# Optimization experiments

Measured on AMD Instinct MI355X. Metric: run time of the kernel, lower is better.

The kernel has to match this reference:

```python
import jax, jax.numpy as jnp
import numpy as np

# FP4 (e2m1) value table: sign bit in code>>3, magnitude in code&7
FP4 = jnp.array([0.0, 0.5, 1.0, 1.5, 2.0, 3.0, 4.0, 6.0,
                 -0.0, -0.5, -1.0, -1.5, -2.0, -3.0, -4.0, -6.0], dtype=jnp.float32)
BLOCK = 32  # MX block size: one shared E8M0 scale per 32 elements


def _unpack(packed):
    # packed: int32 holding byte values 0..255; low nibble first
    lo = packed & 0xF
    hi = (packed >> 4) & 0xF
    return jnp.stack([lo, hi], axis=-1).reshape(*packed.shape[:-1], packed.shape[-1] * 2)


def _dequant(packed, sf):
    # packed: [..., N//2] packed FP4 codes; sf: [..., N//32] E8M0 exponents
    vals = FP4[_unpack(packed)]                       # [..., N]
    n = vals.shape[-1]
    scale = jnp.exp2(sf.astype(jnp.float32) - 127.0)  # [..., N//32]
    vals = vals.reshape(*vals.shape[:-1], n // BLOCK, BLOCK) * scale[..., None]
    return vals.reshape(*scale.shape[:-1], n)


def setup_inputs() -> dict:
    key = jax.random.key(0)
    ks = jax.random.split(key, 6)
    M, IN, OUT, R = 8192, 4096, 4096, 128
    return {
        "x_q": jax.random.randint(ks[0], (M, IN // 2), 0, 256, dtype=jnp.int32),
        "scales_x": jax.random.randint(ks[1], (M, IN // BLOCK), 120, 134, dtype=jnp.int32),
        "weight": jax.random.randint(ks[2], (OUT, IN // 2), 0, 256, dtype=jnp.int32),
        "SF_w": jax.random.randint(ks[3], (OUT * IN // BLOCK,), 120, 134, dtype=jnp.int32),
        "low_rank_weight": jax.random.randint(ks[4], (OUT, R // 2), 0, 256, dtype=jnp.int32),
        "SF_low_rank_weight": jax.random.randint(ks[5], (OUT * R // BLOCK,), 120, 134, dtype=jnp.int32),
    }


def reference(x_q, scales_x, weight, SF_w, low_rank_weight, SF_low_rank_weight):
    OUT = weight.shape[0]
    IN = weight.shape[1] * 2
    R = low_rank_weight.shape[1] * 2  # 128
    # Low-rank path: first R unpacked features of x (R//2 packed bytes, R//32 scale blocks)
    x_lr = _dequant(x_q[:, :R // 2], scales_x[:, :R // BLOCK])                    # [M, R]
    W_lr = _dequant(low_rank_weight, SF_low_rank_weight.reshape(OUT, R // BLOCK))  # [OUT, R]
    out = jnp.einsum('mr,or->mo', x_lr, W_lr, preferred_element_type=jnp.float32)
    # Main 4-bit matmul fused with the low-rank correction
    x = _dequant(x_q, scales_x)                               # [M, IN]
    W = _dequant(weight, SF_w.reshape(OUT, IN // BLOCK))      # [OUT, IN]
    out = out + jnp.einsum('mi,oi->mo', x, W, preferred_element_type=jnp.float32)
    return out
```

## Files before the change

kernel.cpp:

```cpp
#include <hip/hip_runtime.h>
#include <hip/hip_bf16.h>
#include <stdint.h>


#define M_DIM 8192
#define N_DIM 4096
#define K_MAIN 4096
#define K_TOT 4224
#define KB_TOT 2112
#define NT 33

#define XE_OFF   ((size_t)0)
#define WE_OFF   (XE_OFF + (size_t)M_DIM * KB_TOT)
#define SXH_OFF  (WE_OFF + (size_t)N_DIM * KB_TOT)
#define SWH_OFF  (SXH_OFF + (size_t)NT * 2 * M_DIM * 2)
#define WS_NEED  (SWH_OFF + (size_t)NT * 2 * N_DIM * 2)

typedef __attribute__((ext_vector_type(4))) float f32x4;
typedef __attribute__((ext_vector_type(16))) float f32x16;
typedef __attribute__((ext_vector_type(8))) short short8;
typedef __attribute__((ext_vector_type(8))) _Float16 half8;
typedef __attribute__((ext_vector_type(4))) int i32x4;
typedef __attribute__((ext_vector_type(8))) int i32x8;

#define PX_N  (M_DIM * (KB_TOT / 4))
#define PW_N  (N_DIM * (KB_TOT / 4))
#define TSX_N (NT * 2 * M_DIM / 2)
#define TSW_N (NT * 2 * N_DIM / 2)
#define PACK_TOTAL (PX_N + PW_N + TSX_N + TSW_N)

__global__ __launch_bounds__(256)
void pack_kernel(const int* __restrict__ xq, const int* __restrict__ sx,
                 const int* __restrict__ w, const int* __restrict__ sfw,
                 const int* __restrict__ lrw, const int* __restrict__ sflr,
                 uint8_t* __restrict__ ws) {
    int t = blockIdx.x * 256 + threadIdx.x;
    if (t < PX_N) {
        int row = t / (KB_TOT / 4);
        int j = (t % (KB_TOT / 4)) * 4;
        int jsrc = (j < 2048) ? j : (j - 2048);
        i32x4 q = *(const i32x4*)(xq + (size_t)row * 2048 + jsrc);
        unsigned v = (q.x & 255) | ((q.y & 255) << 8) | ((q.z & 255) << 16) |
                     ((unsigned)(q.w & 255) << 24);
        *(unsigned*)(ws + XE_OFF + (size_t)row * KB_TOT + j) = v;
    } else if (t < PX_N + PW_N) {
        int i = t - PX_N;
        int row = i / (KB_TOT / 4);
        int j = (i % (KB_TOT / 4)) * 4;
        i32x4 q;
        if (j < 2048) q = *(const i32x4*)(w + (size_t)row * 2048 + j);
        else          q = *(const i32x4*)(lrw + (size_t)row * 64 + (j - 2048));
        unsigned v = (q.x & 255) | ((q.y & 255) << 8) | ((q.z & 255) << 16) |
                     ((unsigned)(q.w & 255) << 24);
        *(unsigned*)(ws + WE_OFF + (size_t)row * KB_TOT + j) = v;
    } else if (t < PX_N + PW_N + TSX_N) {
        int i = t - PX_N - PW_N;
        int plane = i >> 12;
        int kt = plane >> 1, h = plane & 1;
        int r2 = (i & 4095) << 1;
        int g0 = kt * 4 + h, g2 = g0 + 2;
        int s0 = (g0 < 128) ? g0 : g0 - 128;
        int s2 = (g2 < 128) ? g2 : g2 - 128;
        unsigned b0 = sx[(size_t)r2 * 128 + s0] & 255;
        unsigned b1 = sx[(size_t)r2 * 128 + s2] & 255;
        unsigned b2 = sx[(size_t)(r2 + 1) * 128 + s0] & 255;
        unsigned b3 = sx[(size_t)(r2 + 1) * 128 + s2] & 255;
        *(unsigned*)(ws + SXH_OFF + (size_t)i * 4) = b0 | (b1 << 8) | (b2 << 16) | (b3 << 24);
    } else if (t < PACK_TOTAL) {
        int i = t - PX_N - PW_N - TSX_N;
        int plane = i >> 11;
        int kt = plane >> 1, h = plane & 1;
        int r2 = (i & 2047) << 1;
        int g0 = kt * 4 + h, g2 = g0 + 2;
        unsigned b0, b1, b2, b3;
        if (g0 < 128) { b0 = sfw[(size_t)r2 * 128 + g0] & 255; b2 = sfw[(size_t)(r2 + 1) * 128 + g0] & 255; }
        else          { b0 = sflr[(size_t)r2 * 4 + (g0 - 128)] & 255; b2 = sflr[(size_t)(r2 + 1) * 4 + (g0 - 128)] & 255; }
        if (g2 < 128) { b1 = sfw[(size_t)r2 * 128 + g2] & 255; b3 = sfw[(size_t)(r2 + 1) * 128 + g2] & 255; }
        else          { b1 = sflr[(size_t)r2 * 4 + (g2 - 128)] & 255; b3 = sflr[(size_t)(r2 + 1) * 4 + (g2 - 128)] & 255; }
        *(unsigned*)(ws + SWH_OFF + (size_t)i * 4) = b0 | (b1 << 8) | (b2 << 16) | (b3 << 24);
    }
}

__device__ inline void gload_lds16(const void* g, void* l) {
    __builtin_amdgcn_global_load_lds(
        (const __attribute__((address_space(1))) unsigned int*)g,
        (__attribute__((address_space(3))) unsigned int*)l, 16, 0, 0);
}

__device__ inline void stage_tile(const uint8_t* __restrict__ xe,
                                  const uint8_t* __restrict__ we,
                                  int bm, int bn, int tt,
                                  uint8_t (*As)[256][16], uint8_t (*Bs)[256][16],
                                  int wid, int lane) {
    if (wid < 4) {
        const int c = wid;
        const uint8_t* g = xe + (size_t)(bm + lane) * KB_TOT + tt * 64 + c * 16;
#pragma unroll
        for (int q = 0; q < 4; ++q)
            gload_lds16(g + (size_t)q * 64 * KB_TOT, &As[c][q * 64][0]);
    } else {
        const int c = wid - 4;
        const uint8_t* g = we + (size_t)(bn + lane) * KB_TOT + tt * 64 + c * 16;
#pragma unroll
        for (int q = 0; q < 4; ++q)
            gload_lds16(g + (size_t)q * 64 * KB_TOT, &Bs[c][q * 64][0]);
    }
}

__device__ inline void load_scales(const uint8_t* __restrict__ sxH,
                                   const uint8_t* __restrict__ swH,
                                   int bm, int bn, int tt, int* sa, int* sb,
                                   int wr, int wc, int lane) {
    const int h = lane >> 5, r = lane & 31;
    const uint8_t* px = sxH + (size_t)((tt * 2 + h) * M_DIM + bm + wr * 128 + r) * 2;
#pragma unroll
    for (int mi = 0; mi < 4; ++mi) sa[mi] = *(const unsigned short*)(px + mi * 64);
    const uint8_t* pw = swH + (size_t)((tt * 2 + h) * N_DIM + bn + wc * 64 + r) * 2;
#pragma unroll
    for (int ni = 0; ni < 2; ++ni) sb[ni] = *(const unsigned short*)(pw + ni * 64);
}

template <int KK>
__device__ inline void compute_phase(const uint8_t (*As)[256][16],
                                     const uint8_t (*Bs)[256][16],
                                     f32x16 (&acc)[4][2], const int* sa, const int* sb,
                                     int wr, int wc, int lane) {
    const int h = lane >> 5, r = lane & 31;
    const int c = KK * 2 + h;
    i32x4 af[4], bf[2];
#pragma unroll
    for (int mi = 0; mi < 4; ++mi)
        af[mi] = *(const i32x4*)&As[c][wr * 128 + mi * 32 + r][0];
#pragma unroll
    for (int ni = 0; ni < 2; ++ni)
        bf[ni] = *(const i32x4*)&Bs[c][wc * 64 + ni * 32 + r][0];
    __builtin_amdgcn_s_setprio(1);
#pragma unroll
    for (int mi = 0; mi < 4; ++mi)
#pragma unroll
        for (int ni = 0; ni < 2; ++ni) {
            i32x8 a8 = {af[mi].x, af[mi].y, af[mi].z, af[mi].w, 0, 0, 0, 0};
            i32x8 b8 = {bf[ni].x, bf[ni].y, bf[ni].z, bf[ni].w, 0, 0, 0, 0};
            acc[mi][ni] = __builtin_amdgcn_mfma_scale_f32_32x32x64_f8f6f4(
                a8, b8, acc[mi][ni], 4, 4, KK, sa[mi], KK, sb[ni]);
        }
    __builtin_amdgcn_s_setprio(0);
}

__global__ __launch_bounds__(512, 2)
void l4b_mx2(const uint8_t* __restrict__ xe, const uint8_t* __restrict__ we,
             const uint8_t* __restrict__ sxH, const uint8_t* __restrict__ swH,
             float* __restrict__ out) {
    __shared__ __align__(16) uint8_t As[2][4][256][16];
    __shared__ __align__(16) uint8_t Bs[2][4][256][16];

    const int tid = threadIdx.x;
    const int lane = tid & 63;
    const int wid = tid >> 6;
    const int wr = wid >> 2;
    const int wc = wid & 3;

    const int bid = blockIdx.x;
    const int wgid = (bid & 7) * 64 + (bid >> 3);
    const int bm = (wgid & 31) * 256;
    const int bn = (wgid >> 5) * 256;

    f32x16 acc[4][2] = {};
    int sa[4], sb[2], san[4], sbn[2];

    stage_tile(xe, we, bm, bn, 0, As[0], Bs[0], wid, lane);
    load_scales(sxH, swH, bm, bn, 0, sa, sb, wr, wc, lane);
    __syncthreads();

    int cur = 0;
    for (int t = 0; t < NT - 1; ++t) {
        const int nxt = cur ^ 1;
        stage_tile(xe, we, bm, bn, t + 1, As[nxt], Bs[nxt], wid, lane);
        load_scales(sxH, swH, bm, bn, t + 1, san, sbn, wr, wc, lane);
        compute_phase<0>(As[cur], Bs[cur], acc, sa, sb, wr, wc, lane);
        compute_phase<1>(As[cur], Bs[cur], acc, sa, sb, wr, wc, lane);
        __syncthreads();
        cur = nxt;
#pragma unroll
        for (int i = 0; i < 4; ++i) sa[i] = san[i];
        sb[0] = sbn[0]; sb[1] = sbn[1];
    }
    compute_phase<0>(As[cur], Bs[cur], acc, sa, sb, wr, wc, lane);
    compute_phase<1>(As[cur], Bs[cur], acc, sa, sb, wr, wc, lane);

#pragma unroll
    for (int mi = 0; mi < 4; ++mi)
#pragma unroll
        for (int ni = 0; ni < 2; ++ni) {
            const int col = bn + wc * 64 + ni * 32 + (lane & 31);
            const int rb = bm + wr * 128 + mi * 32 + 4 * (lane >> 5);
#pragma unroll
            for (int reg = 0; reg < 16; ++reg) {
                const int row = rb + (reg & 3) + 8 * (reg >> 2);
                out[(size_t)row * N_DIM + col] = acc[mi][ni][reg];
            }
        }
}

__device__ inline short8 dequant8_f16(i32x4 q, int sf) {
    unsigned b = (unsigned)q.x | ((unsigned)q.y << 8) |
                 ((unsigned)q.z << 16) | ((unsigned)q.w << 24);
    unsigned me = b & 0x07070707u;
    unsigned mo = (b >> 4) & 0x07070707u;
    const unsigned TLO = 0x3E3C3800u;
    const unsigned THI = 0x46444240u;
    unsigned He = __builtin_amdgcn_perm(THI, TLO, me);
    unsigned Ho = __builtin_amdgcn_perm(THI, TLO, mo);
    He |= (b & 0x08080808u) << 4;
    Ho |= (b & 0x80808080u);
    unsigned d0 = __builtin_amdgcn_perm(He, 0u, 0x05010400u);
    unsigned d1 = __builtin_amdgcn_perm(He, 0u, 0x07000600u);
    unsigned d2 = __builtin_amdgcn_perm(Ho, 0u, 0x05010400u);
    unsigned d3 = __builtin_amdgcn_perm(Ho, 0u, 0x07000600u);
    i32x4 di; di.x = (int)d0; di.y = (int)d1; di.z = (int)d2; di.w = (int)d3;
    half8 hh = __builtin_bit_cast(half8, di);
    unsigned short se = (unsigned short)((sf - 112) << 10);
    int srep = (int)((unsigned)se | ((unsigned)se << 16));
    i32x4 si; si.x = srep; si.y = srep; si.z = srep; si.w = srep;
    hh = hh * __builtin_bit_cast(half8, si);
    return __builtin_bit_cast(short8, hh);
}

__global__ __launch_bounds__(256)
void l4b_fused(const int* __restrict__ x_q, const int* __restrict__ scales_x,
               const int* __restrict__ weight, const int* __restrict__ SF_w,
               const int* __restrict__ lrw, const int* __restrict__ SF_lr,
               float* __restrict__ out) {
    __shared__ short As[128 * 64];
    __shared__ short Bs[128 * 64];
    const int tid = threadIdx.x;
    const int lane = tid & 63;
    const int wid = tid >> 6;
    const int wr = wid >> 1, wc = wid & 1;
    const int bm = blockIdx.y * 128, bn = blockIdx.x * 128;
    const int srow = tid >> 3;
    const int scol = (tid & 7) * 8;
    f32x4 acc[4][4] = {};
    for (int kt = 0; kt < K_TOT / 64; ++kt) {
        const int k0 = kt * 64;
        __syncthreads();
#pragma unroll
        for (int it = 0; it < 4; ++it) {
            const int row = it * 32 + srow;
            const int k = k0 + scol;
            const int ksrc = (k < K_MAIN) ? k : (k - K_MAIN);
            i32x4 q = *(const i32x4*)(x_q + (size_t)(bm + row) * 2048 + (ksrc >> 1));
            int sf = scales_x[(size_t)(bm + row) * 128 + (ksrc >> 5)];
            short8 v = dequant8_f16(q, sf);
            unsigned a = (unsigned)(row * 128 + scol * 2) ^ (unsigned)((row & 7) << 4);
            *(short8*)((char*)As + a) = v;
        }
#pragma unroll
        for (int it = 0; it < 4; ++it) {
            const int row = it * 32 + srow;
            const int k = k0 + scol;
            i32x4 q; int sf;
            if (k < K_MAIN) {
                q = *(const i32x4*)(weight + (size_t)(bn + row) * 2048 + (k >> 1));
                sf = SF_w[(size_t)(bn + row) * 128 + (k >> 5)];
            } else {
                q = *(const i32x4*)(lrw + (size_t)(bn + row) * 64 + ((k - K_MAIN) >> 1));
                sf = SF_lr[(size_t)(bn + row) * 4 + ((k - K_MAIN) >> 5)];
            }
            short8 v = dequant8_f16(q, sf);
            unsigned a = (unsigned)(row * 128 + scol * 2) ^ (unsigned)((row & 7) << 4);
            *(short8*)((char*)Bs + a) = v;
        }
        __syncthreads();
#pragma unroll
        for (int ks = 0; ks < 2; ++ks) {
            const int koff = ks * 32 + (lane >> 4) * 8;
            short8 af[4], bfr[4];
#pragma unroll
            for (int mi = 0; mi < 4; ++mi) {
                const int row = wr * 64 + mi * 16 + (lane & 15);
                unsigned a = (unsigned)(row * 128 + koff * 2) ^ (unsigned)((row & 7) << 4);
                af[mi] = *(const short8*)((const char*)As + a);
            }
#pragma unroll
            for (int ni = 0; ni < 4; ++ni) {
                const int row = wc * 64 + ni * 16 + (lane & 15);
                unsigned a = (unsigned)(row * 128 + koff * 2) ^ (unsigned)((row & 7) << 4);
                bfr[ni] = *(const short8*)((const char*)Bs + a);
            }
#pragma unroll
            for (int mi = 0; mi < 4; ++mi)
#pragma unroll
                for (int ni = 0; ni < 4; ++ni)
                    acc[mi][ni] = __builtin_amdgcn_mfma_f32_16x16x32_f16(
                        __builtin_bit_cast(half8, af[mi]),
                        __builtin_bit_cast(half8, bfr[ni]),
                        acc[mi][ni], 0, 0, 0);
        }
    }
#pragma unroll
    for (int mi = 0; mi < 4; ++mi)
#pragma unroll
        for (int ni = 0; ni < 4; ++ni) {
            const int col = bn + wc * 64 + ni * 16 + (lane & 15);
            const int row0 = bm + wr * 64 + mi * 16 + (lane >> 4) * 4;
#pragma unroll
            for (int r2 = 0; r2 < 4; ++r2)
                out[(size_t)(row0 + r2) * N_DIM + col] = acc[mi][ni][r2];
        }
}

extern "C" void kernel_launch(void* const* d_in, const int* in_sizes, int n_in,
                              void* d_out, int out_size, void* d_ws, size_t ws_size,
                              hipStream_t stream) {
    const int* x_q  = (const int*)d_in[0];
    const int* sx   = (const int*)d_in[1];
    const int* w    = (const int*)d_in[2];
    const int* sfw  = (const int*)d_in[3];
    const int* lrw  = (const int*)d_in[4];
    const int* sflr = (const int*)d_in[5];
    float* out = (float*)d_out;

    if (ws_size >= WS_NEED) {
        uint8_t* ws = (uint8_t*)d_ws;
        pack_kernel<<<(PACK_TOTAL + 255) / 256, 256, 0, stream>>>(x_q, sx, w, sfw, lrw, sflr, ws);
        l4b_mx2<<<(M_DIM / 256) * (N_DIM / 256), 512, 0, stream>>>(
            ws + XE_OFF, ws + WE_OFF, ws + SXH_OFF, ws + SWH_OFF, out);
    } else {
        dim3 grid(N_DIM / 128, M_DIM / 128);
        l4b_fused<<<grid, dim3(256), 0, stream>>>(x_q, sx, w, sfw, lrw, sflr, out);
    }
}
```

Before: 139.3 us.

## Repack FP4 operands into chunk-major layout for contiguous tile staging

```diff
diff --git a/kernel.cpp b/kernel.cpp
--- a/kernel.cpp
+++ b/kernel.cpp
@@ -7,12 +7,12 @@
 #define N_DIM 4096
 #define K_MAIN 4096
 #define K_TOT 4224
-#define KB_TOT 2112
+#define NCHUNK 132
 #define NT 33
 
-#define XE_OFF   ((size_t)0)
-#define WE_OFF   (XE_OFF + (size_t)M_DIM * KB_TOT)
-#define SXH_OFF  (WE_OFF + (size_t)N_DIM * KB_TOT)
+#define XP_OFF   ((size_t)0)
+#define WP_OFF   (XP_OFF + (size_t)NCHUNK * M_DIM * 16)
+#define SXH_OFF  (WP_OFF + (size_t)NCHUNK * N_DIM * 16)
 #define SWH_OFF  (SXH_OFF + (size_t)NT * 2 * M_DIM * 2)
 #define WS_NEED  (SWH_OFF + (size_t)NT * 2 * N_DIM * 2)
 
@@ -23,11 +23,16 @@
 typedef __attribute__((ext_vector_type(4))) int i32x4;
 typedef __attribute__((ext_vector_type(8))) int i32x8;
 
-#define PX_N  (M_DIM * (KB_TOT / 4))
-#define PW_N  (N_DIM * (KB_TOT / 4))
+#define PXP_N (NCHUNK * M_DIM)
+#define PWP_N (NCHUNK * N_DIM)
 #define TSX_N (NT * 2 * M_DIM / 2)
 #define TSW_N (NT * 2 * N_DIM / 2)
-#define PACK_TOTAL (PX_N + PW_N + TSX_N + TSW_N)
+#define PACK_TOTAL (PXP_N + PWP_N + TSX_N + TSW_N)
+
+__device__ inline unsigned pack4(i32x4 q) {
+    return (q.x & 255) | ((q.y & 255) << 8) | ((q.z & 255) << 16) |
+           ((unsigned)(q.w & 255) << 24);
+}
 
 __global__ __launch_bounds__(256)
 void pack_kernel(const int* __restrict__ xq, const int* __restrict__ sx,
@@ -35,26 +40,31 @@
                  const int* __restrict__ lrw, const int* __restrict__ sflr,
                  uint8_t* __restrict__ ws) {
     int t = blockIdx.x * 256 + threadIdx.x;
-    if (t < PX_N) {
-        int row = t / (KB_TOT / 4);
-        int j = (t % (KB_TOT / 4)) * 4;
-        int jsrc = (j < 2048) ? j : (j - 2048);
-        i32x4 q = *(const i32x4*)(xq + (size_t)row * 2048 + jsrc);
-        unsigned v = (q.x & 255) | ((q.y & 255) << 8) | ((q.z & 255) << 16) |
-                     ((unsigned)(q.w & 255) << 24);
-        *(unsigned*)(ws + XE_OFF + (size_t)row * KB_TOT + j) = v;
-    } else if (t < PX_N + PW_N) {
-        int i = t - PX_N;
-        int row = i / (KB_TOT / 4);
-        int j = (i % (KB_TOT / 4)) * 4;
-        i32x4 q;
-        if (j < 2048) q = *(const i32x4*)(w + (size_t)row * 2048 + j);
-        else          q = *(const i32x4*)(lrw + (size_t)row * 64 + (j - 2048));
-        unsigned v = (q.x & 255) | ((q.y & 255) << 8) | ((q.z & 255) << 16) |
-                     ((unsigned)(q.w & 255) << 24);
-        *(unsigned*)(ws + WE_OFF + (size_t)row * KB_TOT + j) = v;
-    } else if (t < PX_N + PW_N + TSX_N) {
-        int i = t - PX_N - PW_N;
+    if (t < PXP_N) {
+        const int g = t >> 13;
+        const int m = t & 8191;
+        const int gs = (g < 128) ? g : (g - 128);
+        const int* src = xq + (size_t)m * 2048 + gs * 16;
+        i32x4 o;
+        o.x = (int)pack4(*(const i32x4*)(src + 0));
+        o.y = (int)pack4(*(const i32x4*)(src + 4));
+        o.z = (int)pack4(*(const i32x4*)(src + 8));
+        o.w = (int)pack4(*(const i32x4*)(src + 12));
+        *(i32x4*)(ws + XP_OFF + ((size_t)g * M_DIM + m) * 16) = o;
+    } else if (t < PXP_N + PWP_N) {
+        const int i = t - PXP_N;
+        const int g = i >> 12;
+        const int n = i & 4095;
+        const int* src = (g < 128) ? (w + (size_t)n * 2048 + g * 16)
+                                   : (lrw + (size_t)n * 64 + (g - 128) * 16);
+        i32x4 o;
+        o.x = (int)pack4(*(const i32x4*)(src + 0));
+        o.y = (int)pack4(*(const i32x4*)(src + 4));
+        o.z = (int)pack4(*(const i32x4*)(src + 8));
+        o.w = (int)pack4(*(const i32x4*)(src + 12));
+        *(i32x4*)(ws + WP_OFF + ((size_t)g * N_DIM + n) * 16) = o;
+    } else if (t < PXP_N + PWP_N + TSX_N) {
+        int i = t - PXP_N - PWP_N;
         int plane = i >> 12;
         int kt = plane >> 1, h = plane & 1;
         int r2 = (i & 4095) << 1;
@@ -67,7 +77,7 @@
         unsigned b3 = sx[(size_t)(r2 + 1) * 128 + s2] & 255;
         *(unsigned*)(ws + SXH_OFF + (size_t)i * 4) = b0 | (b1 << 8) | (b2 << 16) | (b3 << 24);
     } else if (t < PACK_TOTAL) {
-        int i = t - PX_N - PW_N - TSX_N;
+        int i = t - PXP_N - PWP_N - TSX_N;
         int plane = i >> 11;
         int kt = plane >> 1, h = plane & 1;
         int r2 = (i & 2047) << 1;
@@ -87,23 +97,22 @@
         (__attribute__((address_space(3))) unsigned int*)l, 16, 0, 0);
 }
 
-__device__ inline void stage_tile(const uint8_t* __restrict__ xe,
-                                  const uint8_t* __restrict__ we,
+__device__ inline void stage_tile(const uint8_t* __restrict__ xp,
+                                  const uint8_t* __restrict__ wp,
                                   int bm, int bn, int tt,
                                   uint8_t (*As)[256][16], uint8_t (*Bs)[256][16],
                                   int wid, int lane) {
+    const int c = wid & 3;
     if (wid < 4) {
-        const int c = wid;
-        const uint8_t* g = xe + (size_t)(bm + lane) * KB_TOT + tt * 64 + c * 16;
+        const uint8_t* g = xp + ((size_t)(tt * 4 + c) * M_DIM + bm + lane) * 16;
 #pragma unroll
         for (int q = 0; q < 4; ++q)
-            gload_lds16(g + (size_t)q * 64 * KB_TOT, &As[c][q * 64][0]);
+            gload_lds16(g + (size_t)q * 64 * 16, &As[c][q * 64][0]);
     } else {
-        const int c = wid - 4;
-        const uint8_t* g = we + (size_t)(bn + lane) * KB_TOT + tt * 64 + c * 16;
+        const uint8_t* g = wp + ((size_t)(tt * 4 + c) * N_DIM + bn + lane) * 16;
 #pragma unroll
         for (int q = 0; q < 4; ++q)
-            gload_lds16(g + (size_t)q * 64 * KB_TOT, &Bs[c][q * 64][0]);
+            gload_lds16(g + (size_t)q * 64 * 16, &Bs[c][q * 64][0]);
     }
 }
 
@@ -148,7 +157,7 @@
 }
 
 __global__ __launch_bounds__(512, 2)
-void l4b_mx2(const uint8_t* __restrict__ xe, const uint8_t* __restrict__ we,
+void l4b_mx3(const uint8_t* __restrict__ xp, const uint8_t* __restrict__ wp,
              const uint8_t* __restrict__ sxH, const uint8_t* __restrict__ swH,
              float* __restrict__ out) {
     __shared__ __align__(16) uint8_t As[2][4][256][16];
@@ -168,14 +177,14 @@
     f32x16 acc[4][2] = {};
     int sa[4], sb[2], san[4], sbn[2];
 
-    stage_tile(xe, we, bm, bn, 0, As[0], Bs[0], wid, lane);
+    stage_tile(xp, wp, bm, bn, 0, As[0], Bs[0], wid, lane);
     load_scales(sxH, swH, bm, bn, 0, sa, sb, wr, wc, lane);
     __syncthreads();
 
     int cur = 0;
     for (int t = 0; t < NT - 1; ++t) {
         const int nxt = cur ^ 1;
-        stage_tile(xe, we, bm, bn, t + 1, As[nxt], Bs[nxt], wid, lane);
+        stage_tile(xp, wp, bm, bn, t + 1, As[nxt], Bs[nxt], wid, lane);
         load_scales(sxH, swH, bm, bn, t + 1, san, sbn, wr, wc, lane);
         compute_phase<0>(As[cur], Bs[cur], acc, sa, sb, wr, wc, lane);
         compute_phase<1>(As[cur], Bs[cur], acc, sa, sb, wr, wc, lane);
@@ -324,8 +333,8 @@
     if (ws_size >= WS_NEED) {
         uint8_t* ws = (uint8_t*)d_ws;
         pack_kernel<<<(PACK_TOTAL + 255) / 256, 256, 0, stream>>>(x_q, sx, w, sfw, lrw, sflr, ws);
-        l4b_mx2<<<(M_DIM / 256) * (N_DIM / 256), 512, 0, stream>>>(
-            ws + XE_OFF, ws + WE_OFF, ws + SXH_OFF, ws + SWH_OFF, out);
+        l4b_mx3<<<(M_DIM / 256) * (N_DIM / 256), 512, 0, stream>>>(
+            ws + XP_OFF, ws + WP_OFF, ws + SXH_OFF, ws + SWH_OFF, out);
     } else {
         dim3 grid(N_DIM / 128, M_DIM / 128);
         l4b_fused<<<grid, dim3(256), 0, stream>>>(x_q, sx, w, sfw, lrw, sflr, out);
```

Result: faster. 119.1 us (-14.5%).
